# Kernel optimization log

Measured on AMD Instinct MI355X. Metric: run time of the kernel, lower is better.

Reference implementation:

```python
import jax, jax.numpy as jnp
import numpy as np

A_CONST = 0.4
C_CONST = 500.0
N_BINS = 10


def entropy(w):
    # Faithful to the torch helper: n=10 half-open bins [min+i*s, min+(i+1)*s);
    # the maximum element falls outside the last bin, as in the original.
    x = w.reshape(-1)
    lo = x.min()
    hi = x.max()
    scale = (hi - lo) / N_BINS
    i = jnp.arange(N_BINS, dtype=x.dtype)
    lower = lo + i * scale            # [n]
    upper = lo + (i + 1.0) * scale    # [n]
    in_bin = (x[None, :] >= lower[:, None]) & (x[None, :] < upper[:, None])  # [n, len]
    p = jnp.sum(in_bin, axis=1).astype(jnp.float32) / x.shape[0]
    return jnp.sum(jnp.where(p > 0, -p * jnp.log(p), 0.0))


def blend_weight(base_w, graft_w, pnet_w):
    # param_direction = |base - graft| passed through bias-free Linear(in, in)
    d = jnp.abs(base_w - graft_w) @ pnet_w.T          # [out, in]
    w_local = jax.nn.sigmoid(d)
    w_global = A_CONST / jnp.pi * jnp.arctan(C_CONST * (entropy(base_w) - entropy(graft_w))) + 0.5
    w_base = w_global * (1.0 - jnp.exp(-w_global * w_local))
    w_graft = (1.0 - w_global) * (1.0 - jnp.exp(-(1.0 - w_global) * (1.0 - w_local)))
    ws = jax.nn.softmax(jnp.stack([w_base, w_graft], axis=-1), axis=-1)  # [out, in, 2]
    return base_w * ws[..., 0] + graft_w * ws[..., 1]


def setup_inputs() -> dict:
    key = jax.random.key(0)
    ks = jax.random.split(key, 9)
    B, D_IN, D_H, D_OUT = 65536, 1024, 512, 1
    return {
        "x": jax.random.normal(ks[0], (B, D_IN), dtype=jnp.float32),
        "w0": jax.random.normal(ks[1], (D_H, D_IN), dtype=jnp.float32) * 0.05,
        "b0": jax.random.normal(ks[2], (D_H,), dtype=jnp.float32) * 0.05,
        "w1": jax.random.normal(ks[3], (D_OUT, D_H), dtype=jnp.float32) * 0.05,
        "b1": jax.random.normal(ks[4], (D_OUT,), dtype=jnp.float32) * 0.05,
        "p0": jax.random.normal(ks[5], (D_IN, D_IN), dtype=jnp.float32) * 0.05,
        "p1": jax.random.normal(ks[6], (D_H, D_H), dtype=jnp.float32) * 0.05,
        "g0": jax.random.normal(ks[7], (D_H, D_IN), dtype=jnp.float32) * 0.05,
        "g1": jax.random.normal(ks[8], (D_OUT, D_H), dtype=jnp.float32) * 0.05,
    }


def reference(x, w0, b0, w1, b1, p0, p1, g0, g1):
    W0 = blend_weight(w0, g0, p0)
    x = jax.nn.relu(x @ W0.T + b0)   # layer 0 + ReLU
    W1 = blend_weight(w1, g1, p1)
    x = x @ W1.T + b1                # layer 1, no activation
    return x
```

## Files before the change

kernel.cpp:

```cpp
#include <hip/hip_runtime.h>
#include <hip/hip_bf16.h>
#include <math.h>


typedef __attribute__((ext_vector_type(8))) short short8;
typedef __attribute__((ext_vector_type(4))) float floatx4;
typedef unsigned short ushort_t;

#define WS_ENT 0
#define WS_MM 4
#define WS_CNT 16
#define WS_W0B_WORD 64
#define WS_W1B_WORD (64 + 262144)

__device__ __forceinline__ unsigned f2ord(float f) {
    unsigned u = __float_as_uint(f);
    return (u & 0x80000000u) ? ~u : (u | 0x80000000u);
}
__device__ __forceinline__ float ord2f(unsigned k) {
    unsigned u = (k & 0x80000000u) ? (k ^ 0x80000000u) : ~k;
    return __uint_as_float(u);
}
__device__ __forceinline__ short f2bf(float f) {
    union { __hip_bfloat16 h; short s; } u;
    u.h = __float2bfloat16(f);
    return u.s;
}
__device__ __forceinline__ float blend_factor(float d, float wg) {
    float wl = 1.0f / (1.0f + expf(-d));
    float wb = wg * (1.0f - expf(-wg * wl));
    float wgr = (1.0f - wg) * (1.0f - expf(-(1.0f - wg) * (1.0f - wl)));
    return 1.0f / (1.0f + expf(-(wb - wgr)));
}
__device__ __forceinline__ float wglobal_from_ent(float eb, float eg) {
    return 0.12732395447351627f * atanf(500.0f * (eb - eg)) + 0.5f;
}
__device__ __forceinline__ void async16(const void* g, void* s) {
    __builtin_amdgcn_global_load_lds(
        (const __attribute__((address_space(1))) unsigned int*)g,
        (__attribute__((address_space(3))) unsigned int*)s, 16, 0, 0);
}

__global__ void init_kernel(unsigned* ws_u, float* out, const float* __restrict__ b1) {
    int gid = blockIdx.x * 256 + threadIdx.x;
    out[gid] = b1[0];
    if (blockIdx.x == 0) {
        int t = threadIdx.x;
        if (t < 4) {
            ws_u[WS_MM + 2 * t] = 0xFFFFFFFFu;
            ws_u[WS_MM + 2 * t + 1] = 0u;
        }
        if (t >= WS_CNT && t < WS_CNT + 40) ws_u[t] = 0u;
    }
}

__device__ __forceinline__ void array_map(int bx, const float* w0, const float* g0,
                                          const float* w1, const float* g1,
                                          int& a, const float*& arr, int& per, int& start) {
    if (bx < 64) { a = 0; arr = w0; per = 524288 / 64; start = bx * per; }
    else if (bx < 128) { a = 1; arr = g0; per = 524288 / 64; start = (bx - 64) * per; }
    else if (bx == 128) { a = 2; arr = w1; per = 512; start = 0; }
    else { a = 3; arr = g1; per = 512; start = 0; }
}

__global__ __launch_bounds__(256) void minmax_kernel(const float* __restrict__ w0,
                                                     const float* __restrict__ g0,
                                                     const float* __restrict__ w1,
                                                     const float* __restrict__ g1,
                                                     unsigned* ws_u) {
    int a, per, start;
    const float* arr;
    array_map(blockIdx.x, w0, g0, w1, g1, a, arr, per, start);
    float mn = INFINITY, mx = -INFINITY;
    for (int i = threadIdx.x; i < per; i += 256) {
        float v = arr[start + i];
        mn = fminf(mn, v);
        mx = fmaxf(mx, v);
    }
#pragma unroll
    for (int off = 32; off > 0; off >>= 1) {
        mn = fminf(mn, __shfl_xor(mn, off));
        mx = fmaxf(mx, __shfl_xor(mx, off));
    }
    __shared__ float smn[4], smx[4];
    int wave = threadIdx.x >> 6, lane = threadIdx.x & 63;
    if (lane == 0) { smn[wave] = mn; smx[wave] = mx; }
    __syncthreads();
    if (threadIdx.x == 0) {
        mn = fminf(fminf(smn[0], smn[1]), fminf(smn[2], smn[3]));
        mx = fmaxf(fmaxf(smx[0], smx[1]), fmaxf(smx[2], smx[3]));
        atomicMin(&ws_u[WS_MM + 2 * a], f2ord(mn));
        atomicMax(&ws_u[WS_MM + 2 * a + 1], f2ord(mx));
    }
}

__global__ __launch_bounds__(256) void hist_kernel(const float* __restrict__ w0,
                                                   const float* __restrict__ g0,
                                                   const float* __restrict__ w1,
                                                   const float* __restrict__ g1,
                                                   unsigned* ws_u) {
    int a, per, start;
    const float* arr;
    array_map(blockIdx.x, w0, g0, w1, g1, a, arr, per, start);
    float lo = ord2f(ws_u[WS_MM + 2 * a]);
    float hi = ord2f(ws_u[WS_MM + 2 * a + 1]);
    float scale = __fdiv_rn(__fsub_rn(hi, lo), 10.0f);
    __shared__ float lower[11];
    __shared__ unsigned cnt[10];
    if (threadIdx.x < 11)
        lower[threadIdx.x] = __fadd_rn(lo, __fmul_rn((float)threadIdx.x, scale));
    if (threadIdx.x < 10) cnt[threadIdx.x] = 0u;
    __syncthreads();
    float inv_scale = 1.0f / scale;
    for (int i = threadIdx.x; i < per; i += 256) {
        float v = arr[start + i];
        int g = (int)floorf((v - lo) * inv_scale);
#pragma unroll
        for (int db = -1; db <= 1; db++) {
            int b = g + db;
            if (b >= 0 && b <= 9 && v >= lower[b] && v < lower[b + 1])
                atomicAdd(&cnt[b], 1u);
        }
    }
    __syncthreads();
    if (threadIdx.x < 10 && cnt[threadIdx.x] > 0)
        atomicAdd(&ws_u[WS_CNT + a * 10 + threadIdx.x], cnt[threadIdx.x]);
}

__global__ void finalize_ent_kernel(unsigned* ws_u) {
    int a = threadIdx.x;
    if (a < 4) {
        float n = (a < 2) ? 524288.0f : 512.0f;
        float ent = 0.0f;
        for (int i = 0; i < 10; i++) {
            float p = __fdiv_rn((float)ws_u[WS_CNT + a * 10 + i], n);
            if (p > 0.0f) ent = __fsub_rn(ent, __fmul_rn(p, logf(p)));
        }
        ((float*)ws_u)[WS_ENT + a] = ent;
    }
}

__global__ __launch_bounds__(256) void blend0_kernel(const float* __restrict__ w0,
                                                     const float* __restrict__ g0,
                                                     const float* __restrict__ p0,
                                                     const float* __restrict__ ws_f,
                                                     ushort_t* __restrict__ W0bb) {
    __shared__ float As[64][17];
    __shared__ float Bs[64][17];
    int tid = threadIdx.x;
    int bo = blockIdx.y * 64;
    int bi = blockIdx.x * 64;
    int tx = tid & 15, ty = tid >> 4;
    int lr = tid >> 2, lc = (tid & 3) * 4;
    float acc[4][4] = {};
    for (int k0 = 0; k0 < 1024; k0 += 16) {
        float4 vw = *(const float4*)&w0[(bo + lr) * 1024 + k0 + lc];
        float4 vg = *(const float4*)&g0[(bo + lr) * 1024 + k0 + lc];
        float4 vp = *(const float4*)&p0[(bi + lr) * 1024 + k0 + lc];
        As[lr][lc + 0] = fabsf(vw.x - vg.x);
        As[lr][lc + 1] = fabsf(vw.y - vg.y);
        As[lr][lc + 2] = fabsf(vw.z - vg.z);
        As[lr][lc + 3] = fabsf(vw.w - vg.w);
        Bs[lr][lc + 0] = vp.x;
        Bs[lr][lc + 1] = vp.y;
        Bs[lr][lc + 2] = vp.z;
        Bs[lr][lc + 3] = vp.w;
        __syncthreads();
#pragma unroll
        for (int k = 0; k < 16; k++) {
            float av[4], bv[4];
#pragma unroll
            for (int r = 0; r < 4; r++) av[r] = As[ty * 4 + r][k];
#pragma unroll
            for (int c = 0; c < 4; c++) bv[c] = Bs[tx * 4 + c][k];
#pragma unroll
            for (int r = 0; r < 4; r++)
#pragma unroll
                for (int c = 0; c < 4; c++) acc[r][c] += av[r] * bv[c];
        }
        __syncthreads();
    }
    float wg = wglobal_from_ent(ws_f[WS_ENT + 0], ws_f[WS_ENT + 1]);
#pragma unroll
    for (int r = 0; r < 4; r++) {
#pragma unroll
        for (int c = 0; c < 4; c++) {
            int o = bo + ty * 4 + r, i = bi + tx * 4 + c;
            float s0 = blend_factor(acc[r][c], wg);
            float v = w0[o * 1024 + i] * s0 + g0[o * 1024 + i] * (1.0f - s0);
            W0bb[o * 1024 + i] = (ushort_t)f2bf(v);
        }
    }
}

__global__ __launch_bounds__(256) void blend1_kernel(const float* __restrict__ w1,
                                                     const float* __restrict__ g1,
                                                     const float* __restrict__ p1,
                                                     const float* __restrict__ ws_f,
                                                     float* __restrict__ W1b) {
    __shared__ float diff[512];
    int tid = threadIdx.x;
    for (int i = tid; i < 512; i += 256) diff[i] = fabsf(w1[i] - g1[i]);
    __syncthreads();
    int wave = tid >> 6, lane = tid & 63;
    int i = blockIdx.x * 4 + wave;
    float acc = 0.0f;
#pragma unroll
    for (int j = 0; j < 8; j++) {
        int k = lane + 64 * j;
        acc += diff[k] * p1[i * 512 + k];
    }
#pragma unroll
    for (int off = 32; off > 0; off >>= 1) acc += __shfl_xor(acc, off);
    if (lane == 0) {
        float wg = wglobal_from_ent(ws_f[WS_ENT + 2], ws_f[WS_ENT + 3]);
        float s0 = blend_factor(acc, wg);
        W1b[i] = w1[i] * s0 + g1[i] * (1.0f - s0);
    }
}

__global__ __launch_bounds__(256) void main_mfma(const float* __restrict__ x,
                                                 const float* __restrict__ b0,
                                                 const ushort_t* __restrict__ W0bb,
                                                 const float* __restrict__ W1b,
                                                 float* __restrict__ out) {
    __shared__ ushort_t As[128 * 40];
    __shared__ ushort_t Bs[128 * 32];
    int tid = threadIdx.x;
    int w = tid >> 6, l = tid & 63;
    int row0 = blockIdx.x * 128, col0 = blockIdx.y * 128;
    int wm = w & 1, wn = w >> 1;
    int m_in = l & 15, kq = l >> 4;

    floatx4 acc[4][4];
    const floatx4 zero = {0.0f, 0.0f, 0.0f, 0.0f};
#pragma unroll
    for (int tm = 0; tm < 4; tm++)
#pragma unroll
        for (int tn = 0; tn < 4; tn++) acc[tm][tn] = zero;

    int arow = tid >> 1;
    int acol = (tid & 1) * 16;
    const float* xbase = x + (size_t)(row0 + arow) * 1024 + acol;
    ushort_t* awr = &As[arow * 40 + acol];
    const ushort_t* bsrc0 = W0bb + (size_t)(col0 + w * 16 + (l >> 2)) * 1024 + (l & 3) * 8;
    const ushort_t* bsrc1 = bsrc0 + (size_t)64 * 1024;
    ushort_t* bdst0 = &Bs[w * 512];
    ushort_t* bdst1 = &Bs[2048 + w * 512];

#pragma unroll 1
    for (int k0 = 0; k0 < 1024; k0 += 32) {
        async16(bsrc0 + k0, bdst0);
        async16(bsrc1 + k0, bdst1);
        float4 v0 = *(const float4*)(xbase + k0);
        float4 v1 = *(const float4*)(xbase + k0 + 4);
        float4 v2 = *(const float4*)(xbase + k0 + 8);
        float4 v3 = *(const float4*)(xbase + k0 + 12);
        short8 s0, s1;
        s0[0] = f2bf(v0.x); s0[1] = f2bf(v0.y); s0[2] = f2bf(v0.z); s0[3] = f2bf(v0.w);
        s0[4] = f2bf(v1.x); s0[5] = f2bf(v1.y); s0[6] = f2bf(v1.z); s0[7] = f2bf(v1.w);
        s1[0] = f2bf(v2.x); s1[1] = f2bf(v2.y); s1[2] = f2bf(v2.z); s1[3] = f2bf(v2.w);
        s1[4] = f2bf(v3.x); s1[5] = f2bf(v3.y); s1[6] = f2bf(v3.z); s1[7] = f2bf(v3.w);
        *(short8*)(awr) = s0;
        *(short8*)(awr + 8) = s1;
        __syncthreads();
        short8 af[4], bfr[4];
#pragma unroll
        for (int tm = 0; tm < 4; tm++)
            af[tm] = *(const short8*)&As[(wm * 64 + tm * 16 + m_in) * 40 + kq * 8];
#pragma unroll
        for (int tn = 0; tn < 4; tn++)
            bfr[tn] = *(const short8*)&Bs[(wn * 64 + tn * 16 + m_in) * 32 + kq * 8];
#pragma unroll
        for (int tm = 0; tm < 4; tm++)
#pragma unroll
            for (int tn = 0; tn < 4; tn++)
                acc[tm][tn] = __builtin_amdgcn_mfma_f32_16x16x32_bf16(
                    af[tm], bfr[tn], acc[tm][tn], 0, 0, 0);
        __syncthreads();
    }

    float b0v[4], w1v[4];
#pragma unroll
    for (int tn = 0; tn < 4; tn++) {
        int h = col0 + wn * 64 + tn * 16 + m_in;
        b0v[tn] = b0[h];
        w1v[tn] = W1b[h];
    }
#pragma unroll
    for (int tm = 0; tm < 4; tm++) {
#pragma unroll
        for (int reg = 0; reg < 4; reg++) {
            float s = 0.0f;
#pragma unroll
            for (int tn = 0; tn < 4; tn++) {
                float y = acc[tm][tn][reg] + b0v[tn];
                y = fmaxf(y, 0.0f);
                s += y * w1v[tn];
            }
            s += __shfl_xor(s, 1);
            s += __shfl_xor(s, 2);
            s += __shfl_xor(s, 4);
            s += __shfl_xor(s, 8);
            if (m_in == 0)
                atomicAdd(&out[row0 + wm * 64 + tm * 16 + kq * 4 + reg], s);
        }
    }
}

extern "C" void kernel_launch(void* const* d_in, const int* in_sizes, int n_in,
                              void* d_out, int out_size, void* d_ws, size_t ws_size,
                              hipStream_t stream) {
    const float* x = (const float*)d_in[0];
    const float* w0 = (const float*)d_in[1];
    const float* b0 = (const float*)d_in[2];
    const float* w1 = (const float*)d_in[3];
    const float* b1 = (const float*)d_in[4];
    const float* p0 = (const float*)d_in[5];
    const float* p1 = (const float*)d_in[6];
    const float* g0 = (const float*)d_in[7];
    const float* g1 = (const float*)d_in[8];
    float* out = (float*)d_out;
    unsigned* ws_u = (unsigned*)d_ws;
    float* ws_f = (float*)d_ws;
    ushort_t* W0bb = (ushort_t*)(ws_u + WS_W0B_WORD);
    float* W1b = ws_f + WS_W1B_WORD;

    init_kernel<<<256, 256, 0, stream>>>(ws_u, out, b1);
    minmax_kernel<<<130, 256, 0, stream>>>(w0, g0, w1, g1, ws_u);
    hist_kernel<<<130, 256, 0, stream>>>(w0, g0, w1, g1, ws_u);
    finalize_ent_kernel<<<1, 64, 0, stream>>>(ws_u);
    blend0_kernel<<<dim3(16, 8), 256, 0, stream>>>(w0, g0, p0, ws_f, W0bb);
    blend1_kernel<<<128, 256, 0, stream>>>(w1, g1, p1, ws_f, W1b);
    main_mfma<<<dim3(512, 4), 256, 0, stream>>>(x, b0, W0bb, W1b, out);
}
```

Before: 628.8 us.

## Retile main GEMM over full hidden width, MFMA blend0, register histogram

The main GEMM now gives each block 64 rows and the full 512-wide hidden dimension. Each x row is therefore read and converted to bf16 once instead of four times, and the per-row output is reduced in LDS and stored directly, with no global atomics and no out-initialisation pass. The next x tile is prefetched into registers, and occupancy is requested at two blocks per CU. blend0 now computes the |w0-g0|·p0ᵀ product with bf16 MFMA instead of fp32 FMA, which lowers the precision of the blend logits. The histogram uses per-thread register counters with wave shuffles instead of LDS atomics. The larger accumulator (128 floats per thread) and a 32 KB B tile raise register and LDS pressure.

```diff
diff --git a/kernel.cpp b/kernel.cpp
--- a/kernel.cpp
+++ b/kernel.cpp
@@ -4,6 +4,7 @@
 
 
 typedef __attribute__((ext_vector_type(8))) short short8;
+typedef __attribute__((ext_vector_type(4))) short short4v;
 typedef __attribute__((ext_vector_type(4))) float floatx4;
 typedef unsigned short ushort_t;
 
@@ -41,17 +42,13 @@
         (__attribute__((address_space(3))) unsigned int*)s, 16, 0, 0);
 }
 
-__global__ void init_kernel(unsigned* ws_u, float* out, const float* __restrict__ b1) {
-    int gid = blockIdx.x * 256 + threadIdx.x;
-    out[gid] = b1[0];
-    if (blockIdx.x == 0) {
-        int t = threadIdx.x;
-        if (t < 4) {
-            ws_u[WS_MM + 2 * t] = 0xFFFFFFFFu;
-            ws_u[WS_MM + 2 * t + 1] = 0u;
-        }
-        if (t >= WS_CNT && t < WS_CNT + 40) ws_u[t] = 0u;
-    }
+__global__ void init_ws(unsigned* ws_u) {
+    int t = threadIdx.x;
+    if (t < 4) {
+        ws_u[WS_MM + 2 * t] = 0xFFFFFFFFu;
+        ws_u[WS_MM + 2 * t + 1] = 0u;
+    }
+    if (t >= WS_CNT && t < WS_CNT + 40) ws_u[t] = 0u;
 }
 
 __device__ __forceinline__ void array_map(int bx, const float* w0, const float* g0,
@@ -105,26 +102,30 @@
     float lo = ord2f(ws_u[WS_MM + 2 * a]);
     float hi = ord2f(ws_u[WS_MM + 2 * a + 1]);
     float scale = __fdiv_rn(__fsub_rn(hi, lo), 10.0f);
-    __shared__ float lower[11];
-    __shared__ unsigned cnt[10];
-    if (threadIdx.x < 11)
-        lower[threadIdx.x] = __fadd_rn(lo, __fmul_rn((float)threadIdx.x, scale));
-    if (threadIdx.x < 10) cnt[threadIdx.x] = 0u;
-    __syncthreads();
-    float inv_scale = 1.0f / scale;
+    float lw[11];
+#pragma unroll
+    for (int j = 0; j < 11; j++)
+        lw[j] = __fadd_rn(lo, __fmul_rn((float)j, scale));
+    unsigned c[10];
+#pragma unroll
+    for (int b = 0; b < 10; b++) c[b] = 0u;
     for (int i = threadIdx.x; i < per; i += 256) {
         float v = arr[start + i];
-        int g = (int)floorf((v - lo) * inv_scale);
-#pragma unroll
-        for (int db = -1; db <= 1; db++) {
-            int b = g + db;
-            if (b >= 0 && b <= 9 && v >= lower[b] && v < lower[b + 1])
-                atomicAdd(&cnt[b], 1u);
-        }
-    }
-    __syncthreads();
-    if (threadIdx.x < 10 && cnt[threadIdx.x] > 0)
-        atomicAdd(&ws_u[WS_CNT + a * 10 + threadIdx.x], cnt[threadIdx.x]);
+#pragma unroll
+        for (int b = 0; b < 10; b++)
+            c[b] += (v >= lw[b] && v < lw[b + 1]) ? 1u : 0u;
+    }
+#pragma unroll
+    for (int b = 0; b < 10; b++) {
+#pragma unroll
+        for (int off = 32; off > 0; off >>= 1) c[b] += __shfl_xor(c[b], off);
+    }
+    int lane = threadIdx.x & 63;
+    if (lane == 0) {
+#pragma unroll
+        for (int b = 0; b < 10; b++)
+            if (c[b] > 0u) atomicAdd(&ws_u[WS_CNT + a * 10 + b], c[b]);
+    }
 }
 
 __global__ void finalize_ent_kernel(unsigned* ws_u) {
@@ -145,48 +146,59 @@
                                                      const float* __restrict__ p0,
                                                      const float* __restrict__ ws_f,
                                                      ushort_t* __restrict__ W0bb) {
-    __shared__ float As[64][17];
-    __shared__ float Bs[64][17];
+    __shared__ ushort_t As[32 * 40];
+    __shared__ ushort_t Ps[64 * 40];
     int tid = threadIdx.x;
-    int bo = blockIdx.y * 64;
+    int w = tid >> 6, l = tid & 63;
+    int bo = blockIdx.y * 32;
     int bi = blockIdx.x * 64;
-    int tx = tid & 15, ty = tid >> 4;
-    int lr = tid >> 2, lc = (tid & 3) * 4;
-    float acc[4][4] = {};
-    for (int k0 = 0; k0 < 1024; k0 += 16) {
-        float4 vw = *(const float4*)&w0[(bo + lr) * 1024 + k0 + lc];
-        float4 vg = *(const float4*)&g0[(bo + lr) * 1024 + k0 + lc];
-        float4 vp = *(const float4*)&p0[(bi + lr) * 1024 + k0 + lc];
-        As[lr][lc + 0] = fabsf(vw.x - vg.x);
-        As[lr][lc + 1] = fabsf(vw.y - vg.y);
-        As[lr][lc + 2] = fabsf(vw.z - vg.z);
-        As[lr][lc + 3] = fabsf(vw.w - vg.w);
-        Bs[lr][lc + 0] = vp.x;
-        Bs[lr][lc + 1] = vp.y;
-        Bs[lr][lc + 2] = vp.z;
-        Bs[lr][lc + 3] = vp.w;
+    int wo = w & 1, wi = w >> 1;
+    int m_in = l & 15, kq = l >> 4;
+
+    floatx4 acc[2];
+    const floatx4 zero = {0.0f, 0.0f, 0.0f, 0.0f};
+    acc[0] = zero; acc[1] = zero;
+
+    int ar = tid >> 3, ac = (tid & 7) * 4;
+    int pr = tid >> 2, pc = (tid & 3) * 8;
+    const float* wbase = w0 + (size_t)(bo + ar) * 1024 + ac;
+    const float* gbase = g0 + (size_t)(bo + ar) * 1024 + ac;
+    const float* pbase = p0 + (size_t)(bi + pr) * 1024 + pc;
+    ushort_t* awr = &As[ar * 40 + ac];
+    ushort_t* pwr = &Ps[pr * 40 + pc];
+
+#pragma unroll 1
+    for (int k0 = 0; k0 < 1024; k0 += 32) {
+        float4 vw = *(const float4*)(wbase + k0);
+        float4 vg = *(const float4*)(gbase + k0);
+        float4 q0 = *(const float4*)(pbase + k0);
+        float4 q1 = *(const float4*)(pbase + k0 + 4);
+        short4v a4;
+        a4[0] = f2bf(fabsf(vw.x - vg.x));
+        a4[1] = f2bf(fabsf(vw.y - vg.y));
+        a4[2] = f2bf(fabsf(vw.z - vg.z));
+        a4[3] = f2bf(fabsf(vw.w - vg.w));
+        short8 p8;
+        p8[0] = f2bf(q0.x); p8[1] = f2bf(q0.y); p8[2] = f2bf(q0.z); p8[3] = f2bf(q0.w);
+        p8[4] = f2bf(q1.x); p8[5] = f2bf(q1.y); p8[6] = f2bf(q1.z); p8[7] = f2bf(q1.w);
+        *(short4v*)awr = a4;
+        *(short8*)pwr = p8;
         __syncthreads();
-#pragma unroll
-        for (int k = 0; k < 16; k++) {
-            float av[4], bv[4];
-#pragma unroll
-            for (int r = 0; r < 4; r++) av[r] = As[ty * 4 + r][k];
-#pragma unroll
-            for (int c = 0; c < 4; c++) bv[c] = Bs[tx * 4 + c][k];
-#pragma unroll
-            for (int r = 0; r < 4; r++)
-#pragma unroll
-                for (int c = 0; c < 4; c++) acc[r][c] += av[r] * bv[c];
-        }
+        short8 af = *(const short8*)&As[(wo * 16 + m_in) * 40 + kq * 8];
+        short8 pf0 = *(const short8*)&Ps[(wi * 32 + m_in) * 40 + kq * 8];
+        short8 pf1 = *(const short8*)&Ps[(wi * 32 + 16 + m_in) * 40 + kq * 8];
+        acc[0] = __builtin_amdgcn_mfma_f32_16x16x32_bf16(af, pf0, acc[0], 0, 0, 0);
+        acc[1] = __builtin_amdgcn_mfma_f32_16x16x32_bf16(af, pf1, acc[1], 0, 0, 0);
         __syncthreads();
     }
     float wg = wglobal_from_ent(ws_f[WS_ENT + 0], ws_f[WS_ENT + 1]);
 #pragma unroll
-    for (int r = 0; r < 4; r++) {
-#pragma unroll
-        for (int c = 0; c < 4; c++) {
-            int o = bo + ty * 4 + r, i = bi + tx * 4 + c;
-            float s0 = blend_factor(acc[r][c], wg);
+    for (int tn = 0; tn < 2; tn++) {
+#pragma unroll
+        for (int reg = 0; reg < 4; reg++) {
+            int o = bo + wo * 16 + kq * 4 + reg;
+            int i = bi + wi * 32 + tn * 16 + m_in;
+            float s0 = blend_factor(acc[tn][reg], wg);
             float v = w0[o * 1024 + i] * s0 + g0[o * 1024 + i] * (1.0f - s0);
             W0bb[o * 1024 + i] = (ushort_t)f2bf(v);
         }
@@ -219,71 +231,68 @@
     }
 }
 
-__global__ __launch_bounds__(256) void main_mfma(const float* __restrict__ x,
-                                                 const float* __restrict__ b0,
-                                                 const ushort_t* __restrict__ W0bb,
-                                                 const float* __restrict__ W1b,
-                                                 float* __restrict__ out) {
-    __shared__ ushort_t As[128 * 40];
-    __shared__ ushort_t Bs[128 * 32];
+__global__ __launch_bounds__(256, 2) void main_mfma(const float* __restrict__ x,
+                                                    const float* __restrict__ b0,
+                                                    const ushort_t* __restrict__ W0bb,
+                                                    const float* __restrict__ W1b,
+                                                    const float* __restrict__ b1,
+                                                    float* __restrict__ out) {
+    __shared__ ushort_t As[64 * 40];
+    __shared__ ushort_t Bs[512 * 32];
+    __shared__ float red[4][64];
     int tid = threadIdx.x;
     int w = tid >> 6, l = tid & 63;
-    int row0 = blockIdx.x * 128, col0 = blockIdx.y * 128;
-    int wm = w & 1, wn = w >> 1;
+    int row0 = blockIdx.x * 64;
     int m_in = l & 15, kq = l >> 4;
 
-    floatx4 acc[4][4];
+    floatx4 acc[4][8];
     const floatx4 zero = {0.0f, 0.0f, 0.0f, 0.0f};
 #pragma unroll
     for (int tm = 0; tm < 4; tm++)
 #pragma unroll
-        for (int tn = 0; tn < 4; tn++) acc[tm][tn] = zero;
-
-    int arow = tid >> 1;
-    int acol = (tid & 1) * 16;
+        for (int tn = 0; tn < 8; tn++) acc[tm][tn] = zero;
+
+    int arow = tid >> 2, acol = (tid & 3) * 8;
     const float* xbase = x + (size_t)(row0 + arow) * 1024 + acol;
     ushort_t* awr = &As[arow * 40 + acol];
-    const ushort_t* bsrc0 = W0bb + (size_t)(col0 + w * 16 + (l >> 2)) * 1024 + (l & 3) * 8;
-    const ushort_t* bsrc1 = bsrc0 + (size_t)64 * 1024;
-    ushort_t* bdst0 = &Bs[w * 512];
-    ushort_t* bdst1 = &Bs[2048 + w * 512];
+    const ushort_t* bsrc = W0bb + (size_t)(w * 16 + (l >> 2)) * 1024 + (l & 3) * 8;
+    ushort_t* bdst = &Bs[w * 512];
+
+    float4 pv0 = *(const float4*)(xbase);
+    float4 pv1 = *(const float4*)(xbase + 4);
 
 #pragma unroll 1
     for (int k0 = 0; k0 < 1024; k0 += 32) {
-        async16(bsrc0 + k0, bdst0);
-        async16(bsrc1 + k0, bdst1);
-        float4 v0 = *(const float4*)(xbase + k0);
-        float4 v1 = *(const float4*)(xbase + k0 + 4);
-        float4 v2 = *(const float4*)(xbase + k0 + 8);
-        float4 v3 = *(const float4*)(xbase + k0 + 12);
-        short8 s0, s1;
-        s0[0] = f2bf(v0.x); s0[1] = f2bf(v0.y); s0[2] = f2bf(v0.z); s0[3] = f2bf(v0.w);
-        s0[4] = f2bf(v1.x); s0[5] = f2bf(v1.y); s0[6] = f2bf(v1.z); s0[7] = f2bf(v1.w);
-        s1[0] = f2bf(v2.x); s1[1] = f2bf(v2.y); s1[2] = f2bf(v2.z); s1[3] = f2bf(v2.w);
-        s1[4] = f2bf(v3.x); s1[5] = f2bf(v3.y); s1[6] = f2bf(v3.z); s1[7] = f2bf(v3.w);
-        *(short8*)(awr) = s0;
-        *(short8*)(awr + 8) = s1;
+#pragma unroll
+        for (int r = 0; r < 8; r++)
+            async16(bsrc + r * 65536 + k0, bdst + r * 2048);
+        short8 s0;
+        s0[0] = f2bf(pv0.x); s0[1] = f2bf(pv0.y); s0[2] = f2bf(pv0.z); s0[3] = f2bf(pv0.w);
+        s0[4] = f2bf(pv1.x); s0[5] = f2bf(pv1.y); s0[6] = f2bf(pv1.z); s0[7] = f2bf(pv1.w);
+        *(short8*)awr = s0;
+        int kn = (k0 + 32 < 1024) ? k0 + 32 : 0;
         __syncthreads();
-        short8 af[4], bfr[4];
+        pv0 = *(const float4*)(xbase + kn);
+        pv1 = *(const float4*)(xbase + kn + 4);
+        short8 af[4];
 #pragma unroll
         for (int tm = 0; tm < 4; tm++)
-            af[tm] = *(const short8*)&As[(wm * 64 + tm * 16 + m_in) * 40 + kq * 8];
-#pragma unroll
-        for (int tn = 0; tn < 4; tn++)
-            bfr[tn] = *(const short8*)&Bs[(wn * 64 + tn * 16 + m_in) * 32 + kq * 8];
-#pragma unroll
-        for (int tm = 0; tm < 4; tm++)
-#pragma unroll
-            for (int tn = 0; tn < 4; tn++)
+            af[tm] = *(const short8*)&As[(tm * 16 + m_in) * 40 + kq * 8];
+#pragma unroll
+        for (int tn = 0; tn < 8; tn++) {
+            short8 bfr = *(const short8*)&Bs[(w * 128 + tn * 16 + m_in) * 32 + kq * 8];
+#pragma unroll
+            for (int tm = 0; tm < 4; tm++)
                 acc[tm][tn] = __builtin_amdgcn_mfma_f32_16x16x32_bf16(
-                    af[tm], bfr[tn], acc[tm][tn], 0, 0, 0);
+                    af[tm], bfr, acc[tm][tn], 0, 0, 0);
+        }
         __syncthreads();
     }
 
-    float b0v[4], w1v[4];
-#pragma unroll
-    for (int tn = 0; tn < 4; tn++) {
-        int h = col0 + wn * 64 + tn * 16 + m_in;
+    float b0v[8], w1v[8];
+#pragma unroll
+    for (int tn = 0; tn < 8; tn++) {
+        int h = w * 128 + tn * 16 + m_in;
         b0v[tn] = b0[h];
         w1v[tn] = W1b[h];
     }
@@ -293,7 +302,7 @@
         for (int reg = 0; reg < 4; reg++) {
             float s = 0.0f;
 #pragma unroll
-            for (int tn = 0; tn < 4; tn++) {
+            for (int tn = 0; tn < 8; tn++) {
                 float y = acc[tm][tn][reg] + b0v[tn];
                 y = fmaxf(y, 0.0f);
                 s += y * w1v[tn];
@@ -302,10 +311,12 @@
             s += __shfl_xor(s, 2);
             s += __shfl_xor(s, 4);
             s += __shfl_xor(s, 8);
-            if (m_in == 0)
-                atomicAdd(&out[row0 + wm * 64 + tm * 16 + kq * 4 + reg], s);
+            if (m_in == 0) red[w][tm * 16 + kq * 4 + reg] = s;
         }
     }
+    __syncthreads();
+    if (tid < 64)
+        out[row0 + tid] = red[0][tid] + red[1][tid] + red[2][tid] + red[3][tid] + b1[0];
 }
 
 extern "C" void kernel_launch(void* const* d_in, const int* in_sizes, int n_in,
@@ -326,11 +337,11 @@
     ushort_t* W0bb = (ushort_t*)(ws_u + WS_W0B_WORD);
     float* W1b = ws_f + WS_W1B_WORD;
 
-    init_kernel<<<256, 256, 0, stream>>>(ws_u, out, b1);
+    init_ws<<<1, 64, 0, stream>>>(ws_u);
     minmax_kernel<<<130, 256, 0, stream>>>(w0, g0, w1, g1, ws_u);
     hist_kernel<<<130, 256, 0, stream>>>(w0, g0, w1, g1, ws_u);
     finalize_ent_kernel<<<1, 64, 0, stream>>>(ws_u);
-    blend0_kernel<<<dim3(16, 8), 256, 0, stream>>>(w0, g0, p0, ws_f, W0bb);
+    blend0_kernel<<<dim3(16, 16), 256, 0, stream>>>(w0, g0, p0, ws_f, W0bb);
     blend1_kernel<<<128, 256, 0, stream>>>(w1, g1, p1, ws_f, W1b);
-    main_mfma<<<dim3(512, 4), 256, 0, stream>>>(x, b0, W0bb, W1b, out);
-}
+    main_mfma<<<1024, 256, 0, stream>>>(x, b0, W0bb, W1b, b1, out);
+}
```

Measured after the change: 525.7 us. -16.4%, faster.
